# Performance work log

Measured on AMD Instinct MI355X. Metric: run time of the kernel, lower is better.

Reference implementation:

```python
import jax, jax.numpy as jnp
import numpy as np

THETA = 10000.0

def _rope(t):
    # lucidrains-style interleaved rotary over the FULL last dim (dim=hidden_size)
    T, d = t.shape[-2], t.shape[-1]
    freqs = 1.0 / (THETA ** (jnp.arange(0, d, 2, dtype=jnp.float32) / d))  # (d/2,)
    ang = jnp.arange(T, dtype=jnp.float32)[:, None] * freqs[None, :]       # (T, d/2)
    ang = jnp.repeat(ang, 2, axis=-1)                                      # (T, d) interleaved
    cos, sin = jnp.cos(ang), jnp.sin(ang)
    x = t.reshape(t.shape[:-1] + (d // 2, 2))
    x1, x2 = x[..., 0], x[..., 1]
    rot = jnp.stack([-x2, x1], axis=-1).reshape(t.shape)  # rotate_half, interleaved pairs
    return t * cos + rot * sin


def setup_inputs() -> dict:
    key = jax.random.key(0)
    ks = jax.random.split(key, 5)
    B, T, C = 4, 2048, 1024
    s = 0.02
    return {
        "x":  jax.random.normal(ks[0], (B, T, C), dtype=jnp.float32),
        "Wq": jax.random.normal(ks[1], (C, C), dtype=jnp.float32) * s,
        "bq": jnp.zeros((C,), dtype=jnp.float32),
        "Wk": jax.random.normal(ks[2], (C, C), dtype=jnp.float32) * s,
        "bk": jnp.zeros((C,), dtype=jnp.float32),
        "Wv": jax.random.normal(ks[3], (C, C), dtype=jnp.float32) * s,
        "bv": jnp.zeros((C,), dtype=jnp.float32),
        "Wf": jax.random.normal(ks[4], (C, C), dtype=jnp.float32) * s,
        "bf": jnp.zeros((C,), dtype=jnp.float32),
    }


def reference(x, Wq, bq, Wk, bk, Wv, bv, Wf, bf):
    B, T, C = x.shape
    Q = _rope(x @ Wq.T + bq)
    K = _rope(x @ Wk.T + bk)
    V = x @ Wv.T + bv
    # scores [B,T,T]; _get_D(gamma=1, T) is exactly a causal lower-triangular mask
    A = jnp.einsum('btd,bsd->bts', Q, K) / jnp.sqrt(jnp.float32(C))
    causal = jnp.tril(jnp.ones((T, T), dtype=bool))
    A = jnp.where(causal, A, -jnp.inf)
    A = jax.nn.softmax(A, axis=-1)
    out = jnp.einsum('bts,bsd->btd', A, V)
    return out @ Wf.T + bf
```

## Files before the change

### kernel.cpp

```cpp
#include <hip/hip_runtime.h>
#include <math.h>


#define AS1(p) ((__attribute__((address_space(1))) void*)(p))
#define AS3(p) ((__attribute__((address_space(3))) void*)(p))

typedef __attribute__((ext_vector_type(8))) short bf16x8;
typedef __attribute__((ext_vector_type(4))) float f32x4;

__device__ __forceinline__ unsigned short f2bf(float f) {
  unsigned int u = __float_as_uint(f);
  u += 0x7fffu + ((u >> 16) & 1u);
  return (unsigned short)(u >> 16);
}

__global__ __launch_bounds__(256) void cast_all(
    const float* __restrict__ x, const float* __restrict__ Wq,
    const float* __restrict__ Wk, const float* __restrict__ Wv,
    const float* __restrict__ Wf,
    unsigned short* __restrict__ xb, unsigned short* __restrict__ Wqb,
    unsigned short* __restrict__ Wkb, unsigned short* __restrict__ Wvb,
    unsigned short* __restrict__ Wfb) {
  int i = blockIdx.x * 256 + threadIdx.x;
  const float* src; unsigned short* dst; int off;
  if (i < 2097152) { src = x; dst = xb; off = i; }
  else {
    int j = i - 2097152;
    int w = j >> 18; off = j & 262143;
    src = (w == 0) ? Wq : (w == 1) ? Wk : (w == 2) ? Wv : Wf;
    dst = (w == 0) ? Wqb : (w == 1) ? Wkb : (w == 2) ? Wvb : Wfb;
  }
  float4 f = ((const float4*)src)[off];
  ushort4 o;
  o.x = f2bf(f.x); o.y = f2bf(f.y); o.z = f2bf(f.z); o.w = f2bf(f.w);
  ((ushort4*)dst)[off] = o;
}

__device__ __forceinline__ void gemm_core(const unsigned short* __restrict__ At, long long lda,
                                          const unsigned short* __restrict__ Bt, long long ldb,
                                          int K, f32x4 (&acc)[4][4],
                                          unsigned short* As, unsigned short* Bs) {
  const int tid  = threadIdx.x;
  const int lane = tid & 63;
  const int w    = tid >> 6;
  const int wm   = (w & 1) << 6;
  const int wn   = (w >> 1) << 6;
  const int fr   = lane & 15;
  const int fq   = lane >> 4;
  const int srow = tid >> 2;
  const int scol = (tid & 3) << 3;
  const int lg   = ((tid & 3) ^ ((srow >> 1) & 3)) << 3;
  const unsigned short* a0 = At + (long long)srow * lda + lg;
  const unsigned short* a1 = At + (long long)(srow + 64) * lda + lg;
  const unsigned short* b0 = Bt + (long long)srow * ldb + lg;
  const unsigned short* b1 = Bt + (long long)(srow + 64) * ldb + lg;
  unsigned short* As0 = As + srow * 32 + scol;
  unsigned short* As1 = As + (srow + 64) * 32 + scol;
  unsigned short* Bs0 = Bs + srow * 32 + scol;
  unsigned short* Bs1 = Bs + (srow + 64) * 32 + scol;
  const int pg = (fq ^ ((fr >> 1) & 3)) << 3;
  for (int k0 = 0; k0 < K; k0 += 32) {
    __builtin_amdgcn_global_load_lds(AS1(a0 + k0), AS3(As0), 16, 0, 0);
    __builtin_amdgcn_global_load_lds(AS1(a1 + k0), AS3(As1), 16, 0, 0);
    __builtin_amdgcn_global_load_lds(AS1(b0 + k0), AS3(Bs0), 16, 0, 0);
    __builtin_amdgcn_global_load_lds(AS1(b1 + k0), AS3(Bs1), 16, 0, 0);
    __syncthreads();
    bf16x8 af[4], bfr[4];
#pragma unroll
    for (int i = 0; i < 4; i++)
      af[i] = *(const bf16x8*)(As + (wm + i * 16 + fr) * 32 + pg);
#pragma unroll
    for (int i = 0; i < 4; i++)
      bfr[i] = *(const bf16x8*)(Bs + (wn + i * 16 + fr) * 32 + pg);
#pragma unroll
    for (int mi = 0; mi < 4; mi++)
#pragma unroll
      for (int ni = 0; ni < 4; ni++)
        acc[mi][ni] = __builtin_amdgcn_mfma_f32_16x16x32_bf16(af[mi], bfr[ni], acc[mi][ni], 0, 0, 0);
    __syncthreads();
  }
}

__device__ __forceinline__ void repack_store_mi(unsigned short (&vals)[4][4],
                                                unsigned short* sh, int mi,
                                                int m0, int n0, long long ldo,
                                                unsigned short* __restrict__ Out) {
  const int tid = threadIdx.x, lane = tid & 63, w = tid >> 6;
  const int half = w & 1, wn = (w >> 1) << 6;
  const int cl = lane & 15, q4 = lane >> 4;
  const int lr = half * 16 + q4 * 4;
#pragma unroll
  for (int ni = 0; ni < 4; ni++)
#pragma unroll
    for (int rr = 0; rr < 4; rr++)
      sh[(lr + rr) * 132 + wn + ni * 16 + cl] = vals[ni][rr];
  __syncthreads();
#pragma unroll
  for (int it = 0; it < 2; ++it) {
    int row = (tid >> 4) + it * 16;
    int c8 = (tid & 15) << 3;
    bf16x8 v = *(const bf16x8*)(sh + row * 132 + c8);
    int gr = m0 + (row < 16 ? mi * 16 + row : 48 + mi * 16 + row);
    *(bf16x8*)(Out + (long long)gr * ldo + n0 + c8) = v;
  }
  __syncthreads();
}

__device__ __forceinline__ void core4(
    const unsigned short* __restrict__ A, long long lda,
    const unsigned short* __restrict__ B, long long ldb,
    int nkt, f32x4 (&acc)[4][4], unsigned short* lds) {
  const int tid  = threadIdx.x;
  const int lane = tid & 63;
  const int w    = tid >> 6;
  const int wr   = w >> 2;
  const int wc   = w & 3;
  const int fr   = lane & 15;
  const int fq   = lane >> 4;
  const int csel = (fq ^ ((fr >> 1) & 3)) << 3;
  const int srow = tid >> 2;
  const int scsw = ((tid & 3) ^ ((srow >> 1) & 3)) << 3;
  const unsigned short* Asrc  = A + (long long)srow * lda + scsw;
  const unsigned short* Bsrc0 = B + (long long)srow * ldb + scsw;
  const unsigned short* Bsrc1 = B + (long long)(srow + 128) * ldb + scsw;
  unsigned short* dsta = lds + tid * 8;

  auto stage = [&](int kt) {
    const int bo = (kt & 3) * 12288;
    const long long ko = (long long)kt * 32;
    __builtin_amdgcn_global_load_lds(AS1(Asrc + ko),  AS3(dsta + bo),        16, 0, 0);
    __builtin_amdgcn_global_load_lds(AS1(Bsrc0 + ko), AS3(dsta + bo + 4096), 16, 0, 0);
    __builtin_amdgcn_global_load_lds(AS1(Bsrc1 + ko), AS3(dsta + bo + 8192), 16, 0, 0);
  };
  auto rdfrag = [&](int kt, bf16x8 (&r)[8]) {
    const unsigned short* Ab = lds + (kt & 3) * 12288 + (wr * 64 + fr) * 32 + csel;
    const unsigned short* Bb = lds + (kt & 3) * 12288 + 4096 + (wc * 64 + fr) * 32 + csel;
#pragma unroll
    for (int mi = 0; mi < 4; ++mi) r[mi] = *(const bf16x8*)(Ab + mi * 512);
#pragma unroll
    for (int nj = 0; nj < 4; ++nj) r[4 + nj] = *(const bf16x8*)(Bb + nj * 512);
  };

  bf16x8 ra[8], rb[8];
  stage(0); stage(1); stage(2);
  asm volatile("s_waitcnt vmcnt(6)" ::: "memory");
  __builtin_amdgcn_s_barrier();
  rdfrag(0, ra);

  auto body = [&](int kt, bf16x8 (&cur)[8], bf16x8 (&nxt)[8]) {
    if (kt + 3 < nkt) {
      stage(kt + 3);
      asm volatile("s_waitcnt vmcnt(6)" ::: "memory");
    } else if (kt + 2 < nkt) {
      asm volatile("s_waitcnt vmcnt(3)" ::: "memory");
    } else if (kt + 1 < nkt) {
      asm volatile("s_waitcnt vmcnt(0)" ::: "memory");
    }
    if (kt + 1 < nkt) {
      __builtin_amdgcn_s_barrier();
      rdfrag(kt + 1, nxt);
    }
    __builtin_amdgcn_s_setprio(1);
#pragma unroll
    for (int mi = 0; mi < 4; ++mi)
#pragma unroll
      for (int nj = 0; nj < 4; ++nj)
        acc[mi][nj] = __builtin_amdgcn_mfma_f32_16x16x32_bf16(cur[mi], cur[4 + nj], acc[mi][nj], 0, 0, 0);
    __builtin_amdgcn_s_setprio(0);
    if (kt + 1 < nkt) __builtin_amdgcn_s_barrier();
  };

#pragma unroll 1
  for (int kt = 0; kt < nkt; kt += 2) {
    body(kt, ra, rb);
    body(kt + 1, rb, ra);
  }
}

__global__ __launch_bounds__(512, 2) void proj_rope(
    const unsigned short* __restrict__ xb,
    const unsigned short* __restrict__ Wq, const unsigned short* __restrict__ Wk,
    const unsigned short* __restrict__ Wv,
    const float* __restrict__ bq, const float* __restrict__ bk, const float* __restrict__ bv,
    unsigned short* __restrict__ Q, unsigned short* __restrict__ Ko,
    unsigned short* __restrict__ Vt) {
  __shared__ unsigned short lds[49152];
  const int which = blockIdx.z;
  const int tid = threadIdx.x, lane = tid & 63, w = tid >> 6;
  const int wr = w >> 2, wc = w & 3;
  const int cl = lane & 15, q4 = lane >> 4;

  f32x4 acc[4][4];
#pragma unroll
  for (int i = 0; i < 4; i++)
#pragma unroll
    for (int j = 0; j < 4; j++)
#pragma unroll
      for (int k = 0; k < 4; k++) acc[i][j][k] = 0.0f;

  if (which == 2) {
    const int p = blockIdx.x + 64 * blockIdx.y;
    const int m0 = ((p >> 3) & 7) * 128;
    const int n0 = (4 * (p & 7) + (p >> 6)) * 256;
    core4(Wv + (long long)m0 * 1024, 1024, xb + (long long)n0 * 1024, 1024, 32, acc, lds);
    __syncthreads();
    const int b = n0 >> 11, sloc = n0 & 2047;
#pragma unroll
    for (int mi = 0; mi < 4; ++mi) {
      const int lr = wr * 64 + mi * 16 + q4 * 4;
#pragma unroll
      for (int rr = 0; rr < 4; ++rr) {
        const float b_ = bv[m0 + lr + rr];
#pragma unroll
        for (int nj = 0; nj < 4; ++nj)
          lds[(lr + rr) * 264 + wc * 64 + nj * 16 + cl] = f2bf(acc[mi][nj][rr] + b_);
      }
    }
    __syncthreads();
    unsigned short* Outb = Vt + (long long)b * 1024 * 2048;
#pragma unroll
    for (int it = 0; it < 8; ++it) {
      int c = it * 512 + tid;
      int row = c >> 5, c8 = (c & 31) << 3;
      bf16x8 v = *(const bf16x8*)(lds + row * 264 + c8);
      *(bf16x8*)(Outb + (long long)(m0 + row) * 2048 + sloc + c8) = v;
    }
    return;
  }

  const int m0 = blockIdx.x * 128;
  const int n0 = blockIdx.y * 256;
  const unsigned short* W = which == 0 ? Wq : Wk;
  const float* bias = which == 0 ? bq : bk;
  unsigned short* Out = which == 0 ? Q : Ko;

  core4(xb + (long long)m0 * 1024, 1024, W + (long long)n0 * 1024, 1024, 32, acc, lds);
  __syncthreads();

  const float NEG_L2T_512 = -0.025952563239354392f;
  const float INV2PI = 0.15915494309189535f;
  float freqn[4];
#pragma unroll
  for (int nj = 0; nj < 4; ++nj) {
    int gn = n0 + wc * 64 + nj * 16 + cl;
    freqn[nj] = exp2f(NEG_L2T_512 * (float)(gn >> 1));
  }
#pragma unroll
  for (int mi = 0; mi < 4; ++mi) {
    const int lr = wr * 64 + mi * 16 + q4 * 4;
    const int t0 = (m0 & 2047) + lr;
#pragma unroll
    for (int nj = 0; nj < 4; ++nj) {
      const int gn = n0 + wc * 64 + nj * 16 + cl;
      const float bi = bias[gn];
#pragma unroll
      for (int rr = 0; rr < 4; ++rr) {
        float v = acc[mi][nj][rr] + bi;
        float partner = __shfl_xor(v, 1, 64);
        float ang = (float)(t0 + rr) * freqn[nj];
        float rev = ang * INV2PI;
        rev = rev - floorf(rev);
        float c_ = __builtin_amdgcn_cosf(rev);
        float s_ = __builtin_amdgcn_sinf(rev);
        v = v * c_ + ((gn & 1) ? partner : -partner) * s_;
        lds[(lr + rr) * 264 + wc * 64 + nj * 16 + cl] = f2bf(v);
      }
    }
  }
  __syncthreads();
#pragma unroll
  for (int it = 0; it < 8; ++it) {
    int c = it * 512 + tid;
    int row = c >> 5, c8 = (c & 31) << 3;
    bf16x8 v = *(const bf16x8*)(lds + row * 264 + c8);
    *(bf16x8*)(Out + (long long)(m0 + row) * 1024 + n0 + c8) = v;
  }
}

__global__ __launch_bounds__(256) void score_exp(const unsigned short* __restrict__ Q,
                                                 const unsigned short* __restrict__ Kk,
                                                 unsigned short* __restrict__ P,
                                                 float* __restrict__ row_sum) {
  __shared__ unsigned short sh[8192];
  const int bx = blockIdx.x;
  int i = (int)((sqrtf(8.0f * (float)bx + 1.0f) - 1.0f) * 0.5f);
  while ((i + 1) * (i + 2) / 2 <= bx) ++i;
  while (i * (i + 1) / 2 > bx) --i;
  const int j = bx - i * (i + 1) / 2;
  const int b = blockIdx.z;
  const int m0 = i * 128, n0 = j * 128;
  const unsigned short* Qb = Q + (long long)b * 2048 * 1024;
  const unsigned short* Kb = Kk + (long long)b * 2048 * 1024;
  unsigned short* Pb = P + (long long)b * 2048 * 2048;
  float* rs = row_sum + b * 2048;

  f32x4 acc[4][4];
#pragma unroll
  for (int ii = 0; ii < 4; ii++)
#pragma unroll
    for (int jj = 0; jj < 4; jj++)
#pragma unroll
      for (int k = 0; k < 4; k++) acc[ii][jj][k] = 0.0f;

  gemm_core(Qb + (long long)m0 * 1024, 1024, Kb + (long long)n0 * 1024, 1024, 1024, acc, sh, sh + 4096);

  const int tid = threadIdx.x, lane = tid & 63, w = tid >> 6;
  const int wm = (w & 1) << 6, wn = (w >> 1) << 6;
  const int cl = lane & 15, q4 = lane >> 4;
  const bool diag = (i == j);
#pragma unroll
  for (int mi = 0; mi < 4; mi++) {
    unsigned short vals[4][4];
    float rsum[4] = {0.f, 0.f, 0.f, 0.f};
#pragma unroll
    for (int ni = 0; ni < 4; ni++) {
      const int gn = n0 + wn + ni * 16 + cl;
#pragma unroll
      for (int rr = 0; rr < 4; rr++) {
        const int gm = m0 + wm + mi * 16 + q4 * 4 + rr;
        float e = (diag && gn > gm) ? 0.0f : __expf(acc[mi][ni][rr] * 0.03125f);
        vals[ni][rr] = f2bf(e);
        rsum[rr] += e;
      }
    }
#pragma unroll
    for (int rr = 0; rr < 4; rr++) {
#pragma unroll
      for (int off = 1; off < 16; off <<= 1) rsum[rr] += __shfl_xor(rsum[rr], off, 64);
    }
    if (cl == 0) {
      const int gm = m0 + wm + mi * 16 + q4 * 4;
#pragma unroll
      for (int rr = 0; rr < 4; rr++) atomicAdd(&rs[gm + rr], rsum[rr]);
    }
    repack_store_mi(vals, sh, mi, m0, n0, 2048, Pb);
  }
}

__global__ __launch_bounds__(256) void pv_gemm(const unsigned short* __restrict__ P,
                                               const unsigned short* __restrict__ Vt,
                                               const float* __restrict__ row_sum,
                                               unsigned short* __restrict__ O) {
  __shared__ unsigned short sh[8192];
  const int b = blockIdx.z;
  const int mt = 15 - blockIdx.x;
  const int m0 = mt * 128;
  const int n0 = blockIdx.y * 128;
  const unsigned short* Pb = P + (long long)b * 2048 * 2048;
  const unsigned short* Vb = Vt + (long long)b * 1024 * 2048;
  const float* rs = row_sum + b * 2048;
  const int K = m0 + 128;

  f32x4 acc[4][4];
#pragma unroll
  for (int i = 0; i < 4; i++)
#pragma unroll
    for (int j = 0; j < 4; j++)
#pragma unroll
      for (int k = 0; k < 4; k++) acc[i][j][k] = 0.0f;

  gemm_core(Pb + (long long)m0 * 2048, 2048, Vb + (long long)n0 * 2048, 2048, K, acc, sh, sh + 4096);

  const int tid = threadIdx.x, lane = tid & 63, w = tid >> 6;
  const int wm = (w & 1) << 6;
  const int q4 = lane >> 4;
#pragma unroll
  for (int mi = 0; mi < 4; mi++) {
    unsigned short vals[4][4];
    float inv[4];
    const int gm0 = m0 + wm + mi * 16 + q4 * 4;
#pragma unroll
    for (int rr = 0; rr < 4; rr++) inv[rr] = 1.0f / rs[gm0 + rr];
#pragma unroll
    for (int ni = 0; ni < 4; ni++)
#pragma unroll
      for (int rr = 0; rr < 4; rr++)
        vals[ni][rr] = f2bf(acc[mi][ni][rr] * inv[rr]);
    repack_store_mi(vals, sh, mi, m0, n0, 1024, O + (long long)b * 2048 * 1024);
  }
}

__global__ __launch_bounds__(512, 2) void final_gemm(const unsigned short* __restrict__ O,
                                                     const unsigned short* __restrict__ Wf,
                                                     const float* __restrict__ bf_,
                                                     float* __restrict__ out) {
  __shared__ unsigned short lds[49152];
  float* shf = (float*)lds;
  const int tid = threadIdx.x, lane = tid & 63, w = tid >> 6;
  const int wr = w >> 2, wc = w & 3;
  const int cl = lane & 15, q4 = lane >> 4;
  const int m0 = blockIdx.x * 128;
  const int n0 = blockIdx.y * 256;

  f32x4 acc[4][4];
#pragma unroll
  for (int i = 0; i < 4; i++)
#pragma unroll
    for (int j = 0; j < 4; j++)
#pragma unroll
      for (int k = 0; k < 4; k++) acc[i][j][k] = 0.0f;

  core4(O + (long long)m0 * 1024, 1024, Wf + (long long)n0 * 1024, 1024, 32, acc, lds);

#pragma unroll
  for (int r = 0; r < 2; ++r) {
    __syncthreads();
    if (wr == r) {
#pragma unroll
      for (int mi = 0; mi < 4; ++mi)
#pragma unroll
        for (int nj = 0; nj < 4; ++nj) {
          const int col = wc * 64 + nj * 16 + cl;
          const float bi = bf_[n0 + col];
#pragma unroll
          for (int rr = 0; rr < 4; ++rr)
            shf[(mi * 16 + q4 * 4 + rr) * 260 + col] = acc[mi][nj][rr] + bi;
        }
    }
    __syncthreads();
#pragma unroll
    for (int it = 0; it < 8; ++it) {
      int c = it * 512 + tid;
      int row = c >> 6, c4 = (c & 63) << 2;
      float4 v = *(const float4*)(shf + row * 260 + c4);
      *(float4*)(out + (long long)(m0 + r * 64 + row) * 1024 + n0 + c4) = v;
    }
  }
}

extern "C" void kernel_launch(void* const* d_in, const int* in_sizes, int n_in,
                              void* d_out, int out_size, void* d_ws, size_t ws_size,
                              hipStream_t stream) {
  (void)in_sizes; (void)n_in; (void)out_size; (void)ws_size;
  const float* x   = (const float*)d_in[0];
  const float* Wq  = (const float*)d_in[1];
  const float* bq  = (const float*)d_in[2];
  const float* Wk  = (const float*)d_in[3];
  const float* bk  = (const float*)d_in[4];
  const float* Wv  = (const float*)d_in[5];
  const float* bv  = (const float*)d_in[6];
  const float* Wf  = (const float*)d_in[7];
  const float* bf_ = (const float*)d_in[8];
  float* out = (float*)d_out;

  char* ws = (char*)d_ws;
  const size_t MB = 1024 * 1024;
  unsigned short* xb  = (unsigned short*)(ws);
  unsigned short* Wqb = (unsigned short*)(ws + 16 * MB);
  unsigned short* Wkb = (unsigned short*)(ws + 18 * MB);
  unsigned short* Wvb = (unsigned short*)(ws + 20 * MB);
  unsigned short* Wfb = (unsigned short*)(ws + 22 * MB);
  unsigned short* Qb  = (unsigned short*)(ws + 24 * MB);
  unsigned short* Kb  = (unsigned short*)(ws + 40 * MB);
  unsigned short* Vtb = (unsigned short*)(ws + 56 * MB);
  unsigned short* Ob  = (unsigned short*)(ws + 72 * MB);
  unsigned short* Pb  = (unsigned short*)(ws + 88 * MB);
  float*          rsum= (float*)(ws + 120 * MB);

  hipMemsetAsync(rsum, 0, 8192 * sizeof(float), stream);
  cast_all<<<dim3(3145728 / 256), dim3(256), 0, stream>>>(x, Wq, Wk, Wv, Wf, xb, Wqb, Wkb, Wvb, Wfb);
  proj_rope<<<dim3(64, 4, 3), dim3(512), 0, stream>>>(xb, Wqb, Wkb, Wvb, bq, bk, bv, Qb, Kb, Vtb);
  score_exp<<<dim3(136, 1, 4), dim3(256), 0, stream>>>(Qb, Kb, Pb, rsum);
  pv_gemm<<<dim3(16, 8, 4), dim3(256), 0, stream>>>(Pb, Vtb, rsum, Ob);
  final_gemm<<<dim3(64, 4), dim3(512), 0, stream>>>(Ob, Wfb, bf_, out);
}
```

Measured before the change: 293.8 us.

## Use 256x256 tiles with 4-stage direct-to-LDS pipeline in projection kernel

Replaces the 128x256 projection GEMM core with a new 256x256 tile core that streams A and B into a four-deep LDS ring via global_load_lds, with explicit vmcnt waits. The launch is flattened to a 1D grid of 384 blocks with a swizzled block-to-tile mapping. The epilogue is split into two halves so the 256-row tile can be written out through LDS. Larger tiles raise arithmetic intensity and halve the block count, but they double the accumulator registers and the LDS footprint (128KB), which likely cuts occupancy despite the launch_bounds(512,2) request.

```diff
diff --git a/kernel.cpp b/kernel.cpp
--- a/kernel.cpp
+++ b/kernel.cpp
@@ -177,6 +177,70 @@
   }
 }
 
+__device__ __forceinline__ void core256(
+    const unsigned short* __restrict__ A, long long lda,
+    const unsigned short* __restrict__ B, long long ldb,
+    int nkt, f32x4 (&acc)[8][4], unsigned short* lds) {
+  const int tid  = threadIdx.x;
+  const int lane = tid & 63;
+  const int w    = tid >> 6;
+  const int wr   = w >> 2;
+  const int wc   = w & 3;
+  const int fr   = lane & 15;
+  const int fq   = lane >> 4;
+  const int csel = (fq ^ ((fr >> 1) & 3)) << 3;
+  const int srow = tid >> 2;
+  const int scsw = ((tid & 3) ^ ((srow >> 1) & 3)) << 3;
+  const unsigned short* As0 = A + (long long)srow * lda + scsw;
+  const unsigned short* As1 = A + (long long)(srow + 128) * lda + scsw;
+  const unsigned short* Bs0 = B + (long long)srow * ldb + scsw;
+  const unsigned short* Bs1 = B + (long long)(srow + 128) * ldb + scsw;
+  unsigned short* dsta = lds + tid * 8;
+
+  auto stage = [&](int kt) {
+    const int bo = (kt & 3) * 16384;
+    const long long ko = (long long)kt * 32;
+    __builtin_amdgcn_global_load_lds(AS1(As0 + ko), AS3(dsta + bo),         16, 0, 0);
+    __builtin_amdgcn_global_load_lds(AS1(As1 + ko), AS3(dsta + bo + 4096),  16, 0, 0);
+    __builtin_amdgcn_global_load_lds(AS1(Bs0 + ko), AS3(dsta + bo + 8192),  16, 0, 0);
+    __builtin_amdgcn_global_load_lds(AS1(Bs1 + ko), AS3(dsta + bo + 12288), 16, 0, 0);
+  };
+
+  stage(0); stage(1); stage(2);
+
+  const unsigned short* Ard = lds + (wr * 128 + fr) * 32 + csel;
+  const unsigned short* Brd = lds + 8192 + (wc * 64 + fr) * 32 + csel;
+
+#pragma unroll 1
+  for (int kt = 0; kt < nkt; ++kt) {
+    if (kt + 3 < nkt) {
+      stage(kt + 3);
+      asm volatile("s_waitcnt vmcnt(12)" ::: "memory");
+    } else if (kt + 2 < nkt) {
+      asm volatile("s_waitcnt vmcnt(8)" ::: "memory");
+    } else if (kt + 1 < nkt) {
+      asm volatile("s_waitcnt vmcnt(4)" ::: "memory");
+    } else {
+      asm volatile("s_waitcnt vmcnt(0)" ::: "memory");
+    }
+    __builtin_amdgcn_s_barrier();
+    const int bo = (kt & 3) * 16384;
+    bf16x8 b4[4], a8[8];
+#pragma unroll
+    for (int nj = 0; nj < 4; ++nj) b4[nj] = *(const bf16x8*)(Brd + bo + nj * 512);
+#pragma unroll
+    for (int mi = 0; mi < 8; ++mi) a8[mi] = *(const bf16x8*)(Ard + bo + mi * 512);
+    __builtin_amdgcn_s_setprio(1);
+#pragma unroll
+    for (int mi = 0; mi < 8; ++mi)
+#pragma unroll
+      for (int nj = 0; nj < 4; ++nj)
+        acc[mi][nj] = __builtin_amdgcn_mfma_f32_16x16x32_bf16(a8[mi], b4[nj], acc[mi][nj], 0, 0, 0);
+    __builtin_amdgcn_s_setprio(0);
+    __builtin_amdgcn_s_barrier();
+  }
+}
+
 __global__ __launch_bounds__(512, 2) void proj_rope(
     const unsigned short* __restrict__ xb,
     const unsigned short* __restrict__ Wq, const unsigned short* __restrict__ Wk,
@@ -184,96 +248,108 @@
     const float* __restrict__ bq, const float* __restrict__ bk, const float* __restrict__ bv,
     unsigned short* __restrict__ Q, unsigned short* __restrict__ Ko,
     unsigned short* __restrict__ Vt) {
-  __shared__ unsigned short lds[49152];
-  const int which = blockIdx.z;
+  __shared__ unsigned short lds[65536];
+  const int bid = blockIdx.x;
+  const int swz = (bid & 7) * 48 + (bid >> 3);
+  const int which = swz >> 7;
+  const int t = swz & 127;
   const int tid = threadIdx.x, lane = tid & 63, w = tid >> 6;
   const int wr = w >> 2, wc = w & 3;
   const int cl = lane & 15, q4 = lane >> 4;
 
-  f32x4 acc[4][4];
-#pragma unroll
-  for (int i = 0; i < 4; i++)
+  f32x4 acc[8][4];
+#pragma unroll
+  for (int i = 0; i < 8; i++)
 #pragma unroll
     for (int j = 0; j < 4; j++)
 #pragma unroll
       for (int k = 0; k < 4; k++) acc[i][j][k] = 0.0f;
 
   if (which == 2) {
-    const int p = blockIdx.x + 64 * blockIdx.y;
-    const int m0 = ((p >> 3) & 7) * 128;
-    const int n0 = (4 * (p & 7) + (p >> 6)) * 256;
-    core4(Wv + (long long)m0 * 1024, 1024, xb + (long long)n0 * 1024, 1024, 32, acc, lds);
+    const int m0 = (t & 3) * 256;
+    const int n0 = (t >> 2) * 256;
+    core256(Wv + (long long)m0 * 1024, 1024, xb + (long long)n0 * 1024, 1024, 32, acc, lds);
+    const int b = n0 >> 11, sloc = n0 & 2047;
+    unsigned short* Outb = Vt + (long long)b * 1024 * 2048;
+#pragma unroll
+    for (int r = 0; r < 2; ++r) {
+      __syncthreads();
+      if (wr == r) {
+#pragma unroll
+        for (int mi = 0; mi < 8; ++mi) {
+          const int lr = mi * 16 + q4 * 4;
+#pragma unroll
+          for (int rr = 0; rr < 4; ++rr) {
+            const float b_ = bv[m0 + r * 128 + lr + rr];
+#pragma unroll
+            for (int nj = 0; nj < 4; ++nj)
+              lds[(lr + rr) * 264 + wc * 64 + nj * 16 + cl] = f2bf(acc[mi][nj][rr] + b_);
+          }
+        }
+      }
+      __syncthreads();
+#pragma unroll
+      for (int it = 0; it < 8; ++it) {
+        int c = it * 512 + tid;
+        int row = c >> 5, c8 = (c & 31) << 3;
+        bf16x8 v = *(const bf16x8*)(lds + row * 264 + c8);
+        *(bf16x8*)(Outb + (long long)(m0 + r * 128 + row) * 2048 + sloc + c8) = v;
+      }
+    }
+    return;
+  }
+
+  const int m0 = (t >> 2) * 256;
+  const int n0 = (t & 3) * 256;
+  const unsigned short* W = which == 0 ? Wq : Wk;
+  const float* bias = which == 0 ? bq : bk;
+  unsigned short* Out = which == 0 ? Q : Ko;
+
+  core256(xb + (long long)m0 * 1024, 1024, W + (long long)n0 * 1024, 1024, 32, acc, lds);
+
+  const float NEG_L2T_512 = -0.025952563239354392f;
+  const float INV2PI = 0.15915494309189535f;
+  float freqn[4];
+#pragma unroll
+  for (int nj = 0; nj < 4; ++nj) {
+    int gn = n0 + wc * 64 + nj * 16 + cl;
+    freqn[nj] = exp2f(NEG_L2T_512 * (float)(gn >> 1));
+  }
+#pragma unroll
+  for (int r = 0; r < 2; ++r) {
     __syncthreads();
-    const int b = n0 >> 11, sloc = n0 & 2047;
-#pragma unroll
-    for (int mi = 0; mi < 4; ++mi) {
-      const int lr = wr * 64 + mi * 16 + q4 * 4;
-#pragma unroll
-      for (int rr = 0; rr < 4; ++rr) {
-        const float b_ = bv[m0 + lr + rr];
-#pragma unroll
-        for (int nj = 0; nj < 4; ++nj)
-          lds[(lr + rr) * 264 + wc * 64 + nj * 16 + cl] = f2bf(acc[mi][nj][rr] + b_);
+    if (wr == r) {
+#pragma unroll
+      for (int mi = 0; mi < 8; ++mi) {
+        const int lr = mi * 16 + q4 * 4;
+        const int t0 = ((m0 + r * 128) & 2047) + lr;
+#pragma unroll
+        for (int nj = 0; nj < 4; ++nj) {
+          const int gn = n0 + wc * 64 + nj * 16 + cl;
+          const float bi = bias[gn];
+#pragma unroll
+          for (int rr = 0; rr < 4; ++rr) {
+            float v = acc[mi][nj][rr] + bi;
+            float partner = __shfl_xor(v, 1, 64);
+            float ang = (float)(t0 + rr) * freqn[nj];
+            float rev = ang * INV2PI;
+            rev = rev - floorf(rev);
+            float c_ = __builtin_amdgcn_cosf(rev);
+            float s_ = __builtin_amdgcn_sinf(rev);
+            v = v * c_ + ((gn & 1) ? partner : -partner) * s_;
+            lds[(lr + rr) * 264 + wc * 64 + nj * 16 + cl] = f2bf(v);
+          }
+        }
       }
     }
     __syncthreads();
-    unsigned short* Outb = Vt + (long long)b * 1024 * 2048;
 #pragma unroll
     for (int it = 0; it < 8; ++it) {
       int c = it * 512 + tid;
       int row = c >> 5, c8 = (c & 31) << 3;
       bf16x8 v = *(const bf16x8*)(lds + row * 264 + c8);
-      *(bf16x8*)(Outb + (long long)(m0 + row) * 2048 + sloc + c8) = v;
-    }
-    return;
-  }
-
-  const int m0 = blockIdx.x * 128;
-  const int n0 = blockIdx.y * 256;
-  const unsigned short* W = which == 0 ? Wq : Wk;
-  const float* bias = which == 0 ? bq : bk;
-  unsigned short* Out = which == 0 ? Q : Ko;
-
-  core4(xb + (long long)m0 * 1024, 1024, W + (long long)n0 * 1024, 1024, 32, acc, lds);
-  __syncthreads();
-
-  const float NEG_L2T_512 = -0.025952563239354392f;
-  const float INV2PI = 0.15915494309189535f;
-  float freqn[4];
-#pragma unroll
-  for (int nj = 0; nj < 4; ++nj) {
-    int gn = n0 + wc * 64 + nj * 16 + cl;
-    freqn[nj] = exp2f(NEG_L2T_512 * (float)(gn >> 1));
-  }
-#pragma unroll
-  for (int mi = 0; mi < 4; ++mi) {
-    const int lr = wr * 64 + mi * 16 + q4 * 4;
-    const int t0 = (m0 & 2047) + lr;
-#pragma unroll
-    for (int nj = 0; nj < 4; ++nj) {
-      const int gn = n0 + wc * 64 + nj * 16 + cl;
-      const float bi = bias[gn];
-#pragma unroll
-      for (int rr = 0; rr < 4; ++rr) {
-        float v = acc[mi][nj][rr] + bi;
-        float partner = __shfl_xor(v, 1, 64);
-        float ang = (float)(t0 + rr) * freqn[nj];
-        float rev = ang * INV2PI;
-        rev = rev - floorf(rev);
-        float c_ = __builtin_amdgcn_cosf(rev);
-        float s_ = __builtin_amdgcn_sinf(rev);
-        v = v * c_ + ((gn & 1) ? partner : -partner) * s_;
-        lds[(lr + rr) * 264 + wc * 64 + nj * 16 + cl] = f2bf(v);
-      }
-    }
-  }
-  __syncthreads();
-#pragma unroll
-  for (int it = 0; it < 8; ++it) {
-    int c = it * 512 + tid;
-    int row = c >> 5, c8 = (c & 31) << 3;
-    bf16x8 v = *(const bf16x8*)(lds + row * 264 + c8);
-    *(bf16x8*)(Out + (long long)(m0 + row) * 1024 + n0 + c8) = v;
+      *(bf16x8*)(Out + (long long)(m0 + r * 128 + row) * 1024 + n0 + c8) = v;
+    }
   }
 }
 
@@ -459,7 +535,7 @@
 
   hipMemsetAsync(rsum, 0, 8192 * sizeof(float), stream);
   cast_all<<<dim3(3145728 / 256), dim3(256), 0, stream>>>(x, Wq, Wk, Wv, Wf, xb, Wqb, Wkb, Wvb, Wfb);
-  proj_rope<<<dim3(64, 4, 3), dim3(512), 0, stream>>>(xb, Wqb, Wkb, Wvb, bq, bk, bv, Qb, Kb, Vtb);
+  proj_rope<<<dim3(384), dim3(512), 0, stream>>>(xb, Wqb, Wkb, Wvb, bq, bk, bv, Qb, Kb, Vtb);
   score_exp<<<dim3(136, 1, 4), dim3(256), 0, stream>>>(Qb, Kb, Pb, rsum);
   pv_gemm<<<dim3(16, 8, 4), dim3(256), 0, stream>>>(Pb, Vtb, rsum, Ob);
   final_gemm<<<dim3(64, 4), dim3(512), 0, stream>>>(Ob, Wfb, bf_, out);
```

Result: slower. 316.6 us (+7.8%).

## Replace single-buffered GEMM core with 4-stage async LDS pipeline in attention kernels

Applied to the files above, without the earlier changes.

Swaps the simple load-sync-compute loop used by score_exp and pv_gemm for a 4-buffer ring of global_load_lds stages. Loads run three k-tiles ahead, and the next tile's fragments are read into registers while the current tile's MFMAs issue at raised priority. This aims to hide global memory latency and remove one barrier per iteration. In exchange, LDS per block grows fourfold to 64KB, with launch bounds set to two blocks per CU, and correctness now depends on hand-written vmcnt waits.

```diff
diff --git a/kernel.cpp b/kernel.cpp
--- a/kernel.cpp
+++ b/kernel.cpp
@@ -34,51 +34,6 @@
   ushort4 o;
   o.x = f2bf(f.x); o.y = f2bf(f.y); o.z = f2bf(f.z); o.w = f2bf(f.w);
   ((ushort4*)dst)[off] = o;
-}
-
-__device__ __forceinline__ void gemm_core(const unsigned short* __restrict__ At, long long lda,
-                                          const unsigned short* __restrict__ Bt, long long ldb,
-                                          int K, f32x4 (&acc)[4][4],
-                                          unsigned short* As, unsigned short* Bs) {
-  const int tid  = threadIdx.x;
-  const int lane = tid & 63;
-  const int w    = tid >> 6;
-  const int wm   = (w & 1) << 6;
-  const int wn   = (w >> 1) << 6;
-  const int fr   = lane & 15;
-  const int fq   = lane >> 4;
-  const int srow = tid >> 2;
-  const int scol = (tid & 3) << 3;
-  const int lg   = ((tid & 3) ^ ((srow >> 1) & 3)) << 3;
-  const unsigned short* a0 = At + (long long)srow * lda + lg;
-  const unsigned short* a1 = At + (long long)(srow + 64) * lda + lg;
-  const unsigned short* b0 = Bt + (long long)srow * ldb + lg;
-  const unsigned short* b1 = Bt + (long long)(srow + 64) * ldb + lg;
-  unsigned short* As0 = As + srow * 32 + scol;
-  unsigned short* As1 = As + (srow + 64) * 32 + scol;
-  unsigned short* Bs0 = Bs + srow * 32 + scol;
-  unsigned short* Bs1 = Bs + (srow + 64) * 32 + scol;
-  const int pg = (fq ^ ((fr >> 1) & 3)) << 3;
-  for (int k0 = 0; k0 < K; k0 += 32) {
-    __builtin_amdgcn_global_load_lds(AS1(a0 + k0), AS3(As0), 16, 0, 0);
-    __builtin_amdgcn_global_load_lds(AS1(a1 + k0), AS3(As1), 16, 0, 0);
-    __builtin_amdgcn_global_load_lds(AS1(b0 + k0), AS3(Bs0), 16, 0, 0);
-    __builtin_amdgcn_global_load_lds(AS1(b1 + k0), AS3(Bs1), 16, 0, 0);
-    __syncthreads();
-    bf16x8 af[4], bfr[4];
-#pragma unroll
-    for (int i = 0; i < 4; i++)
-      af[i] = *(const bf16x8*)(As + (wm + i * 16 + fr) * 32 + pg);
-#pragma unroll
-    for (int i = 0; i < 4; i++)
-      bfr[i] = *(const bf16x8*)(Bs + (wn + i * 16 + fr) * 32 + pg);
-#pragma unroll
-    for (int mi = 0; mi < 4; mi++)
-#pragma unroll
-      for (int ni = 0; ni < 4; ni++)
-        acc[mi][ni] = __builtin_amdgcn_mfma_f32_16x16x32_bf16(af[mi], bfr[ni], acc[mi][ni], 0, 0, 0);
-    __syncthreads();
-  }
 }
 
 __device__ __forceinline__ void repack_store_mi(unsigned short (&vals)[4][4],
@@ -177,6 +132,79 @@
   }
 }
 
+__device__ __forceinline__ void core4h(
+    const unsigned short* __restrict__ A, long long lda,
+    const unsigned short* __restrict__ B, long long ldb,
+    int nkt, f32x4 (&acc)[4][4], unsigned short* lds) {
+  const int tid  = threadIdx.x;
+  const int lane = tid & 63;
+  const int w    = tid >> 6;
+  const int wm   = (w & 1) << 6;
+  const int wn   = (w >> 1) << 6;
+  const int fr   = lane & 15;
+  const int fq   = lane >> 4;
+  const int csel = (fq ^ ((fr >> 1) & 3)) << 3;
+  const int srow = tid >> 2;
+  const int scsw = ((tid & 3) ^ ((srow >> 1) & 3)) << 3;
+  const unsigned short* Asrc0 = A + (long long)srow * lda + scsw;
+  const unsigned short* Asrc1 = A + (long long)(srow + 64) * lda + scsw;
+  const unsigned short* Bsrc0 = B + (long long)srow * ldb + scsw;
+  const unsigned short* Bsrc1 = B + (long long)(srow + 64) * ldb + scsw;
+  unsigned short* dsta = lds + tid * 8;
+
+  auto stage = [&](int kt) {
+    const int bo = (kt & 3) * 8192;
+    const long long ko = (long long)kt * 32;
+    __builtin_amdgcn_global_load_lds(AS1(Asrc0 + ko), AS3(dsta + bo),        16, 0, 0);
+    __builtin_amdgcn_global_load_lds(AS1(Asrc1 + ko), AS3(dsta + bo + 2048), 16, 0, 0);
+    __builtin_amdgcn_global_load_lds(AS1(Bsrc0 + ko), AS3(dsta + bo + 4096), 16, 0, 0);
+    __builtin_amdgcn_global_load_lds(AS1(Bsrc1 + ko), AS3(dsta + bo + 6144), 16, 0, 0);
+  };
+  auto rdfrag = [&](int kt, bf16x8 (&r)[8]) {
+    const unsigned short* Ab = lds + (kt & 3) * 8192 + (wm + fr) * 32 + csel;
+    const unsigned short* Bb = lds + (kt & 3) * 8192 + 4096 + (wn + fr) * 32 + csel;
+#pragma unroll
+    for (int mi = 0; mi < 4; ++mi) r[mi] = *(const bf16x8*)(Ab + mi * 512);
+#pragma unroll
+    for (int nj = 0; nj < 4; ++nj) r[4 + nj] = *(const bf16x8*)(Bb + nj * 512);
+  };
+
+  bf16x8 ra[8], rb[8];
+  stage(0); stage(1); stage(2);
+  asm volatile("s_waitcnt vmcnt(8)" ::: "memory");
+  __builtin_amdgcn_s_barrier();
+  rdfrag(0, ra);
+
+  auto body = [&](int kt, bf16x8 (&cur)[8], bf16x8 (&nxt)[8]) {
+    if (kt + 3 < nkt) {
+      stage(kt + 3);
+      asm volatile("s_waitcnt vmcnt(8)" ::: "memory");
+    } else if (kt + 2 < nkt) {
+      asm volatile("s_waitcnt vmcnt(4)" ::: "memory");
+    } else if (kt + 1 < nkt) {
+      asm volatile("s_waitcnt vmcnt(0)" ::: "memory");
+    }
+    if (kt + 1 < nkt) {
+      __builtin_amdgcn_s_barrier();
+      rdfrag(kt + 1, nxt);
+    }
+    __builtin_amdgcn_s_setprio(1);
+#pragma unroll
+    for (int mi = 0; mi < 4; ++mi)
+#pragma unroll
+      for (int nj = 0; nj < 4; ++nj)
+        acc[mi][nj] = __builtin_amdgcn_mfma_f32_16x16x32_bf16(cur[mi], cur[4 + nj], acc[mi][nj], 0, 0, 0);
+    __builtin_amdgcn_s_setprio(0);
+    if (kt + 1 < nkt) __builtin_amdgcn_s_barrier();
+  };
+
+#pragma unroll 1
+  for (int kt = 0; kt < nkt; kt += 2) {
+    body(kt, ra, rb);
+    body(kt + 1, rb, ra);
+  }
+}
+
 __global__ __launch_bounds__(512, 2) void proj_rope(
     const unsigned short* __restrict__ xb,
     const unsigned short* __restrict__ Wq, const unsigned short* __restrict__ Wk,
@@ -277,11 +305,11 @@
   }
 }
 
-__global__ __launch_bounds__(256) void score_exp(const unsigned short* __restrict__ Q,
-                                                 const unsigned short* __restrict__ Kk,
-                                                 unsigned short* __restrict__ P,
-                                                 float* __restrict__ row_sum) {
-  __shared__ unsigned short sh[8192];
+__global__ __launch_bounds__(256, 2) void score_exp(const unsigned short* __restrict__ Q,
+                                                    const unsigned short* __restrict__ Kk,
+                                                    unsigned short* __restrict__ P,
+                                                    float* __restrict__ row_sum) {
+  __shared__ unsigned short sh[32768];
   const int bx = blockIdx.x;
   int i = (int)((sqrtf(8.0f * (float)bx + 1.0f) - 1.0f) * 0.5f);
   while ((i + 1) * (i + 2) / 2 <= bx) ++i;
@@ -302,7 +330,8 @@
 #pragma unroll
       for (int k = 0; k < 4; k++) acc[ii][jj][k] = 0.0f;
 
-  gemm_core(Qb + (long long)m0 * 1024, 1024, Kb + (long long)n0 * 1024, 1024, 1024, acc, sh, sh + 4096);
+  core4h(Qb + (long long)m0 * 1024, 1024, Kb + (long long)n0 * 1024, 1024, 32, acc, sh);
+  __syncthreads();
 
   const int tid = threadIdx.x, lane = tid & 63, w = tid >> 6;
   const int wm = (w & 1) << 6, wn = (w >> 1) << 6;
@@ -337,11 +366,11 @@
   }
 }
 
-__global__ __launch_bounds__(256) void pv_gemm(const unsigned short* __restrict__ P,
-                                               const unsigned short* __restrict__ Vt,
-                                               const float* __restrict__ row_sum,
-                                               unsigned short* __restrict__ O) {
-  __shared__ unsigned short sh[8192];
+__global__ __launch_bounds__(256, 2) void pv_gemm(const unsigned short* __restrict__ P,
+                                                  const unsigned short* __restrict__ Vt,
+                                                  const float* __restrict__ row_sum,
+                                                  unsigned short* __restrict__ O) {
+  __shared__ unsigned short sh[32768];
   const int b = blockIdx.z;
   const int mt = 15 - blockIdx.x;
   const int m0 = mt * 128;
@@ -349,7 +378,7 @@
   const unsigned short* Pb = P + (long long)b * 2048 * 2048;
   const unsigned short* Vb = Vt + (long long)b * 1024 * 2048;
   const float* rs = row_sum + b * 2048;
-  const int K = m0 + 128;
+  const int nkt = 4 * (mt + 1);
 
   f32x4 acc[4][4];
 #pragma unroll
@@ -359,7 +388,8 @@
 #pragma unroll
       for (int k = 0; k < 4; k++) acc[i][j][k] = 0.0f;
 
-  gemm_core(Pb + (long long)m0 * 2048, 2048, Vb + (long long)n0 * 2048, 2048, K, acc, sh, sh + 4096);
+  core4h(Pb + (long long)m0 * 2048, 2048, Vb + (long long)n0 * 2048, 2048, nkt, acc, sh);
+  __syncthreads();
 
   const int tid = threadIdx.x, lane = tid & 63, w = tid >> 6;
   const int wm = (w & 1) << 6;
```

New measurement: 290.2 us. About the same (-1.2%).
